# Performance work log

Measured on AMD Instinct MI355X. Metric: run time of the kernel, lower is better.

The kernel has to match this reference:

```python
import jax, jax.numpy as jnp
import numpy as np

B, S, D, E, T = 16, 128, 128, 64, 128  # batch, seq_len, token_dim, dep_dim, transformed_dim (T==D required by mask broadcast)
V_TOK, V_DEP = 100000, 64
DEPTH = 2


def setup_inputs() -> dict:
    key = jax.random.key(0)
    ks = jax.random.split(key, 12)
    return {
        "token_table": jax.random.normal(ks[0], (V_TOK, D), jnp.float32) * 0.1,
        "dep_table": jax.random.normal(ks[1], (V_DEP, E), jnp.float32) * 0.1,
        # Bilinear(D, E, T): weight [T, D, E], bias [T]
        "W1": jax.random.normal(ks[2], (T, D, E), jnp.float32) * 0.05,
        "b1": jax.random.normal(ks[3], (T,), jnp.float32) * 0.05,
        # Bilinear(D, T, D): weight [D, D, T], bias [D]
        "W2": jax.random.normal(ks[4], (D, D, T), jnp.float32) * 0.05,
        "b2": jax.random.normal(ks[5], (D,), jnp.float32) * 0.05,
        # Linear(S, 1): weight [S] (flattened [1,S]), bias [1]
        "wr": jax.random.normal(ks[6], (S,), jnp.float32) * 0.05,
        "br": jax.random.normal(ks[7], (1,), jnp.float32) * 0.05,
        "tokens": jax.random.randint(ks[8], (B, S), 0, V_TOK),
        "dep_types": jax.random.randint(ks[9], (B, S), 0, V_DEP),
        "dep_heads": jax.random.randint(ks[10], (B, S), 0, S),
    }


def _block(tok, dep_emb, heads, W1, b1, W2, b2, wr, br):
    # tok: [B,S,D], dep_emb: [B,S,E], heads: [B,S] with values in [0,S)
    b, s, d = tok.shape
    # dep_transform (Bilinear) + mask + tanh. Masked structure: full tensor
    # tde_full[b,i,j,:] = tde[b,j,:] if heads[b,j]==i else 0 (heads<S always here),
    # and tanh(0)=0, so only the i==heads[b,j] rows are nonzero after activation.
    tde = jnp.tanh(jnp.einsum('bsd,tde,bse->bst', tok, W1, dep_emb) + b1)  # [B,S,T]
    # composition bilinear at the nonzero (i==head) positions
    c_nz = jnp.tanh(jnp.einsum('bsd,pdt,bst->bsp', tok, W2, tde) + b2)    # [B,S,D]
    # at masked positions tde_full==0 -> composition output is tanh(bias)
    c_bg = jnp.tanh(b2)                                                   # [D]
    # reduction Linear(S,1): out[b,i,:] = sum_j wr[j]*c[b,i,j,:] + br
    base = jnp.sum(wr) * c_bg + br                                        # [D]
    delta = wr[None, :, None] * (c_nz - c_bg)                             # [B,S,D]
    seg = (jnp.arange(b)[:, None] * s + heads).reshape(-1)                # scatter target i=heads[b,j]
    scat = jax.ops.segment_sum(delta.reshape(b * s, d), seg, num_segments=b * s)
    return base + scat.reshape(b, s, d)


def reference(token_table, dep_table, W1, b1, W2, b2, wr, br, tokens, dep_types, dep_heads):
    tok = token_table[tokens]          # [B,S,D]
    dep = dep_table[dep_types]         # [B,S,E]
    for _ in range(DEPTH):
        tok = _block(tok, dep, dep_heads, W1, b1, W2, b2, wr, br)
    out_mask = (dep_heads == 0)[..., None].astype(tok.dtype)  # keep only root tokens
    return tok * out_mask
```

## Files before the change

### kernel.cpp

```cpp
#include <hip/hip_runtime.h>
#include <hip/hip_bf16.h>

#define BB 16
#define SS 128
#define DD 128
#define EE 64
#define TT 128
#define NN (BB*SS)
#define KSPLIT 16

typedef __attribute__((ext_vector_type(8))) short short8;
typedef __attribute__((ext_vector_type(4))) float f32x4;
typedef __attribute__((ext_vector_type(4))) unsigned int u32x4;

__device__ inline unsigned pkbf16(float a, float b) {
    unsigned r;
    asm volatile("v_cvt_pk_bf16_f32 %0, %1, %2" : "=v"(r) : "v"(a), "v"(b));
    return r;
}
__device__ inline float bflo(unsigned u) { return __builtin_bit_cast(float, (unsigned)(u << 16)); }
__device__ inline float bfhi(unsigned u) { return __builtin_bit_cast(float, (unsigned)(u & 0xffff0000u)); }

#define LDS_SWZ(row, bcol) ((row) * 256 + ((bcol) ^ (((row) & 7) << 4)))

__global__ __launch_bounds__(256) void k_prep1(const float* __restrict__ W1,
                                               const float* __restrict__ dep_table,
                                               const float* __restrict__ W2,
                                               const float* __restrict__ b2,
                                               const float* __restrict__ wr,
                                               const float* __restrict__ br,
                                               __hip_bfloat16* __restrict__ G1,
                                               __hip_bfloat16* __restrict__ W2b,
                                               float* __restrict__ basics) {
    int bid = blockIdx.x;
    int tid = threadIdx.x;
    if (bid < 512) {
        int bx = bid & 63, by = bid >> 6;
        int td = bx * 256 + tid;
        int v0 = by * 8;
        const float* w1row = W1 + (size_t)td * 64;
        float acc[8] = {};
#pragma unroll
        for (int e0 = 0; e0 < 64; e0 += 8) {
            f32x4 wa = *(const f32x4*)(w1row + e0);
            f32x4 wb = *(const f32x4*)(w1row + e0 + 4);
#pragma unroll
            for (int v = 0; v < 8; v++) {
                const float* dr = dep_table + (v0 + v) * 64 + e0;
                acc[v] += wa[0] * dr[0] + wa[1] * dr[1] + wa[2] * dr[2] + wa[3] * dr[3]
                        + wb[0] * dr[4] + wb[1] * dr[5] + wb[2] * dr[6] + wb[3] * dr[7];
            }
        }
#pragma unroll
        for (int v = 0; v < 8; v++)
            G1[(size_t)(v0 + v) * (TT * DD) + td] = __float2bfloat16(acc[v]);
    } else if (bid < 1536) {
        int cid = (bid - 512) * 256 + tid;
        int d = cid >> 11;
        int rem = cid & 2047;
        int p = rem >> 4;
        int sp = rem & 15;
        int h = sp >> 3, s = sp & 7;
        int t0 = h * 64 + ((s ^ (p & 7))) * 8;
        const float* src = W2 + ((size_t)p * 128 + d) * 128 + t0;
        f32x4 a = *(const f32x4*)(src);
        f32x4 b = *(const f32x4*)(src + 4);
        u32x4 o;
        o[0] = pkbf16(a[0], a[1]);
        o[1] = pkbf16(a[2], a[3]);
        o[2] = pkbf16(b[0], b[1]);
        o[3] = pkbf16(b[2], b[3]);
        *(u32x4*)((char*)W2b + (size_t)cid * 16) = o;
    } else {
        __shared__ float red[128];
        int t = tid;
        if (t < 128) red[t] = wr[t];
        __syncthreads();
        for (int s = 64; s > 0; s >>= 1) {
            if (t < s) red[t] += red[t + s];
            __syncthreads();
        }
        if (t < 128) {
            float swr = red[0];
            float cbg = tanhf(b2[t]);
            basics[t] = cbg;
            basics[128 + t] = swr * cbg + br[0];
        }
    }
}

__global__ __launch_bounds__(256) void k_prep2(const float* __restrict__ token_table,
                                               const int* __restrict__ tokens,
                                               const int* __restrict__ dep_types,
                                               const float* __restrict__ b1,
                                               const __hip_bfloat16* __restrict__ G1,
                                               float* __restrict__ tok,
                                               float* __restrict__ tde) {
    __shared__ float rows[2][128];
    int tid = threadIdx.x;
    int gid = blockIdx.x * 256 + tid;
    int n = gid >> 7, t = tid & 127, half = tid >> 7;
    float val = token_table[(size_t)tokens[n] * 128 + t];
    tok[gid] = val;
    rows[half][t] = val;
    __syncthreads();
    int v = dep_types[n];
    const unsigned* g = (const unsigned*)(G1 + (size_t)v * (TT * DD) + t * 128);
    const float* row = rows[half];
    float acc = b1[t];
#pragma unroll
    for (int i = 0; i < 16; i++) {
        u32x4 w = *(const u32x4*)(g + i * 4);
        acc += row[i * 8 + 0] * bflo(w[0]) + row[i * 8 + 1] * bfhi(w[0]);
        acc += row[i * 8 + 2] * bflo(w[1]) + row[i * 8 + 3] * bfhi(w[1]);
        acc += row[i * 8 + 4] * bflo(w[2]) + row[i * 8 + 5] * bfhi(w[2]);
        acc += row[i * 8 + 6] * bflo(w[3]) + row[i * 8 + 7] * bfhi(w[3]);
    }
    tde[(size_t)n * 128 + t] = tanhf(acc);
}

__global__ __launch_bounds__(256, 4) void k_gemm(const float* __restrict__ tok,
                                                 const float* __restrict__ tde,
                                                 const __hip_bfloat16* __restrict__ W2b,
                                                 float* __restrict__ part) {
    __shared__ char As[8192];
    __shared__ char Bs[32768];
    int id = blockIdx.x;
    int g = id & 7;
    int rblk = id >> 3;
    int ks = g * 2 + (rblk & 1);
    int nb = rblk >> 1;
    int tid = threadIdx.x;
    int lane = tid & 63, w = tid >> 6;
    int n0 = nb * 32, d0 = ks * 8;
    int lrow = lane & 15, lk = lane >> 4;
    int r = tid >> 3, o = tid & 7;
    int wbase16 = (tid & 192) * 16;

    f32x4 acc[2][2] = {};

    for (int dd = 0; dd < 8; dd++) {
        int d = d0 + dd;
        const char* bsrc = (const char*)W2b + (size_t)d * 32768;
#pragma unroll
        for (int i = 0; i < 8; i++) {
            __builtin_amdgcn_global_load_lds(
                (const __attribute__((address_space(1))) void*)(bsrc + (i * 256 + tid) * 16),
                (__attribute__((address_space(3))) void*)(Bs + i * 4096 + wbase16),
                16, 0, 0);
        }
        float tokv = tok[(size_t)(n0 + r) * 128 + d];
        const float* trow = tde + (size_t)(n0 + r) * 128 + o * 16;
        f32x4 xa = *(const f32x4*)(trow);
        f32x4 xb = *(const f32x4*)(trow + 4);
        f32x4 ya = *(const f32x4*)(trow + 8);
        f32x4 yb = *(const f32x4*)(trow + 12);
        u32x4 v0, v1;
        v0[0] = pkbf16(xa[0] * tokv, xa[1] * tokv);
        v0[1] = pkbf16(xa[2] * tokv, xa[3] * tokv);
        v0[2] = pkbf16(xb[0] * tokv, xb[1] * tokv);
        v0[3] = pkbf16(xb[2] * tokv, xb[3] * tokv);
        v1[0] = pkbf16(ya[0] * tokv, ya[1] * tokv);
        v1[1] = pkbf16(ya[2] * tokv, ya[3] * tokv);
        v1[2] = pkbf16(yb[0] * tokv, yb[1] * tokv);
        v1[3] = pkbf16(yb[2] * tokv, yb[3] * tokv);
        *(u32x4*)(As + LDS_SWZ(r, o * 32))      = v0;
        *(u32x4*)(As + LDS_SWZ(r, o * 32 + 16)) = v1;
        __syncthreads();
#pragma unroll
        for (int kk = 0; kk < 4; kk++) {
            short8 aF[2], bF[2];
#pragma unroll
            for (int mi = 0; mi < 2; mi++)
                aF[mi] = *(const short8*)(As + LDS_SWZ(mi * 16 + lrow, kk * 64 + lk * 16));
#pragma unroll
            for (int pj = 0; pj < 2; pj++)
                bF[pj] = *(const short8*)(Bs + LDS_SWZ(w * 32 + pj * 16 + lrow, kk * 64 + lk * 16));
#pragma unroll
            for (int mi = 0; mi < 2; mi++)
#pragma unroll
                for (int pj = 0; pj < 2; pj++)
                    acc[mi][pj] = __builtin_amdgcn_mfma_f32_16x16x32_bf16(
                        aF[mi], bF[pj], acc[mi][pj], 0, 0, 0);
        }
        __syncthreads();
    }
    float* pout = part + (size_t)ks * NN * 128;
#pragma unroll
    for (int mi = 0; mi < 2; mi++)
#pragma unroll
        for (int pj = 0; pj < 2; pj++)
#pragma unroll
            for (int rr = 0; rr < 4; rr++) {
                int row = mi * 16 + (lane >> 4) * 4 + rr;
                int col = w * 32 + pj * 16 + (lane & 15);
                pout[(size_t)(n0 + row) * 128 + col] = acc[mi][pj][rr];
            }
}

__global__ void k_e2a(const float* __restrict__ part, const int* __restrict__ heads,
                      const float* __restrict__ basics, const float* __restrict__ wr,
                      const float* __restrict__ b2, const int* __restrict__ dep_types,
                      const float* __restrict__ b1, const __hip_bfloat16* __restrict__ G1,
                      float* __restrict__ tok, float* __restrict__ tde) {
    int bi = blockIdx.x;
    int b = bi >> 7, i = bi & 127;
    int p = threadIdx.x;
    __shared__ int hs[128];
    __shared__ float row[128];
    hs[p] = heads[b * 128 + p];
    __syncthreads();
    float cbg = basics[p];
    float acc = basics[128 + p];
    for (int j = 0; j < 128; j++) {
        if (hs[j] == i) {
            int gg = (b * 128 + j) * 128 + p;
            float s = 0.f;
#pragma unroll
            for (int k = 0; k < KSPLIT; k++) s += part[(size_t)k * NN * 128 + gg];
            float c = tanhf(s + b2[p]);
            acc += wr[j] * (c - cbg);
        }
    }
    tok[(size_t)bi * 128 + p] = acc;
    row[p] = acc;
    __syncthreads();
    int v = dep_types[bi];
    const unsigned* g = (const unsigned*)(G1 + (size_t)v * (TT * DD) + p * 128);
    float a2 = b1[p];
#pragma unroll
    for (int ii = 0; ii < 16; ii++) {
        u32x4 w = *(const u32x4*)(g + ii * 4);
        a2 += row[ii * 8 + 0] * bflo(w[0]) + row[ii * 8 + 1] * bfhi(w[0]);
        a2 += row[ii * 8 + 2] * bflo(w[1]) + row[ii * 8 + 3] * bfhi(w[1]);
        a2 += row[ii * 8 + 4] * bflo(w[2]) + row[ii * 8 + 5] * bfhi(w[2]);
        a2 += row[ii * 8 + 6] * bflo(w[3]) + row[ii * 8 + 7] * bfhi(w[3]);
    }
    tde[(size_t)bi * 128 + p] = tanhf(a2);
}

__global__ void k_e2b(const float* __restrict__ part, const int* __restrict__ heads,
                      const float* __restrict__ basics, const float* __restrict__ wr,
                      const float* __restrict__ b2, float* __restrict__ out) {
    int bi = blockIdx.x;
    int b = bi >> 7, i = bi & 127;
    int p = threadIdx.x;
    __shared__ int hs[128];
    hs[p] = heads[b * 128 + p];
    __syncthreads();
    if (hs[i] != 0) {
        out[(size_t)bi * 128 + p] = 0.f;
        return;
    }
    float cbg = basics[p];
    float acc = basics[128 + p];
    for (int j = 0; j < 128; j++) {
        if (hs[j] == i) {
            int gg = (b * 128 + j) * 128 + p;
            float s = 0.f;
#pragma unroll
            for (int k = 0; k < KSPLIT; k++) s += part[(size_t)k * NN * 128 + gg];
            float c = tanhf(s + b2[p]);
            acc += wr[j] * (c - cbg);
        }
    }
    out[(size_t)bi * 128 + p] = acc;
}

extern "C" void kernel_launch(void* const* d_in, const int* in_sizes, int n_in,
                              void* d_out, int out_size, void* d_ws, size_t ws_size,
                              hipStream_t stream) {
    const float* token_table = (const float*)d_in[0];
    const float* dep_table   = (const float*)d_in[1];
    const float* W1          = (const float*)d_in[2];
    const float* b1          = (const float*)d_in[3];
    const float* W2          = (const float*)d_in[4];
    const float* b2          = (const float*)d_in[5];
    const float* wr          = (const float*)d_in[6];
    const float* br          = (const float*)d_in[7];
    const int* tokens        = (const int*)d_in[8];
    const int* dep_types     = (const int*)d_in[9];
    const int* dep_heads     = (const int*)d_in[10];
    float* out = (float*)d_out;

    char* ws = (char*)d_ws;
    __hip_bfloat16* G1  = (__hip_bfloat16*)(ws);
    __hip_bfloat16* W2b = (__hip_bfloat16*)(ws + (2ull << 20));
    float* tok    = (float*)(ws + (6ull << 20));
    float* tde    = (float*)(ws + (7ull << 20));
    float* part   = (float*)(ws + (9ull << 20));
    float* basics = (float*)(ws + (25ull << 20));

    k_prep1<<<1537, 256, 0, stream>>>(W1, dep_table, W2, b2, wr, br, G1, W2b, basics);
    k_prep2<<<1024, 256, 0, stream>>>(token_table, tokens, dep_types, b1, G1, tok, tde);

    k_gemm<<<1024, 256, 0, stream>>>(tok, tde, W2b, part);
    k_e2a<<<NN, 128, 0, stream>>>(part, dep_heads, basics, wr, b2,
                                  dep_types, b1, G1, tok, tde);
    k_gemm<<<1024, 256, 0, stream>>>(tok, tde, W2b, part);
    k_e2b<<<NN, 128, 0, stream>>>(part, dep_heads, basics, wr, b2, out);
}
```

Before: 105.0 us.

## Drop LDS staging in composition GEMM; load MFMA fragments directly from pre-permuted weights

The W2 bf16 repack is changed to write weights in MFMA-fragment order, so each lane loads its B operand with one contiguous 16-byte global load. The GEMM kernel no longer stages A and B through shared memory or uses barriers. Each wave keeps its tde rows in registers and builds the A fragments itself by scaling them with the token value. The block-to-tile mapping is also simplified. This removes LDS traffic and __syncthreads, but every wave now reads its B fragments straight from global memory or cache, and the extra tde registers may lower occupancy.

```diff
diff --git a/kernel.cpp b/kernel.cpp
--- a/kernel.cpp
+++ b/kernel.cpp
@@ -20,8 +20,6 @@
 }
 __device__ inline float bflo(unsigned u) { return __builtin_bit_cast(float, (unsigned)(u << 16)); }
 __device__ inline float bfhi(unsigned u) { return __builtin_bit_cast(float, (unsigned)(u & 0xffff0000u)); }
-
-#define LDS_SWZ(row, bcol) ((row) * 256 + ((bcol) ^ (((row) & 7) << 4)))
 
 __global__ __launch_bounds__(256) void k_prep1(const float* __restrict__ W1,
                                                const float* __restrict__ dep_table,
@@ -56,12 +54,12 @@
             G1[(size_t)(v0 + v) * (TT * DD) + td] = __float2bfloat16(acc[v]);
     } else if (bid < 1536) {
         int cid = (bid - 512) * 256 + tid;
-        int d = cid >> 11;
-        int rem = cid & 2047;
-        int p = rem >> 4;
-        int sp = rem & 15;
-        int h = sp >> 3, s = sp & 7;
-        int t0 = h * 64 + ((s ^ (p & 7))) * 8;
+        int l  = cid & 63;
+        int pf = (cid >> 6) & 7;
+        int kk = (cid >> 9) & 3;
+        int d  = cid >> 11;
+        int p  = pf * 16 + (l & 15);
+        int t0 = kk * 32 + (l >> 4) * 8;
         const float* src = W2 + ((size_t)p * 128 + d) * 128 + t0;
         f32x4 a = *(const f32x4*)(src);
         f32x4 b = *(const f32x4*)(src + 4);
@@ -123,67 +121,54 @@
                                                  const float* __restrict__ tde,
                                                  const __hip_bfloat16* __restrict__ W2b,
                                                  float* __restrict__ part) {
-    __shared__ char As[8192];
-    __shared__ char Bs[32768];
-    int id = blockIdx.x;
-    int g = id & 7;
-    int rblk = id >> 3;
-    int ks = g * 2 + (rblk & 1);
-    int nb = rblk >> 1;
     int tid = threadIdx.x;
-    int lane = tid & 63, w = tid >> 6;
-    int n0 = nb * 32, d0 = ks * 8;
-    int lrow = lane & 15, lk = lane >> 4;
-    int r = tid >> 3, o = tid & 7;
-    int wbase16 = (tid & 192) * 16;
+    int w = tid >> 6, lane = tid & 63;
+    int nt = blockIdx.x & 63, ks = blockIdx.x >> 6;
+    int n0 = nt * 32, d0 = ks * 8;
+    int lr = lane & 15, lk = lane >> 4;
+
+    f32x4 ta[2][4], tb[2][4];
+#pragma unroll
+    for (int mi = 0; mi < 2; mi++) {
+        const float* base = tde + (size_t)(n0 + mi * 16 + lr) * 128 + lk * 8;
+#pragma unroll
+        for (int kk = 0; kk < 4; kk++) {
+            ta[mi][kk] = *(const f32x4*)(base + kk * 32);
+            tb[mi][kk] = *(const f32x4*)(base + kk * 32 + 4);
+        }
+    }
+    const float* tokp0 = tok + (size_t)(n0 + lr) * 128 + d0;
+    const float* tokp1 = tok + (size_t)(n0 + 16 + lr) * 128 + d0;
 
     f32x4 acc[2][2] = {};
-
+    const char* wb = (const char*)W2b;
+
+#pragma unroll 2
     for (int dd = 0; dd < 8; dd++) {
         int d = d0 + dd;
-        const char* bsrc = (const char*)W2b + (size_t)d * 32768;
-#pragma unroll
-        for (int i = 0; i < 8; i++) {
-            __builtin_amdgcn_global_load_lds(
-                (const __attribute__((address_space(1))) void*)(bsrc + (i * 256 + tid) * 16),
-                (__attribute__((address_space(3))) void*)(Bs + i * 4096 + wbase16),
-                16, 0, 0);
-        }
-        float tokv = tok[(size_t)(n0 + r) * 128 + d];
-        const float* trow = tde + (size_t)(n0 + r) * 128 + o * 16;
-        f32x4 xa = *(const f32x4*)(trow);
-        f32x4 xb = *(const f32x4*)(trow + 4);
-        f32x4 ya = *(const f32x4*)(trow + 8);
-        f32x4 yb = *(const f32x4*)(trow + 12);
-        u32x4 v0, v1;
-        v0[0] = pkbf16(xa[0] * tokv, xa[1] * tokv);
-        v0[1] = pkbf16(xa[2] * tokv, xa[3] * tokv);
-        v0[2] = pkbf16(xb[0] * tokv, xb[1] * tokv);
-        v0[3] = pkbf16(xb[2] * tokv, xb[3] * tokv);
-        v1[0] = pkbf16(ya[0] * tokv, ya[1] * tokv);
-        v1[1] = pkbf16(ya[2] * tokv, ya[3] * tokv);
-        v1[2] = pkbf16(yb[0] * tokv, yb[1] * tokv);
-        v1[3] = pkbf16(yb[2] * tokv, yb[3] * tokv);
-        *(u32x4*)(As + LDS_SWZ(r, o * 32))      = v0;
-        *(u32x4*)(As + LDS_SWZ(r, o * 32 + 16)) = v1;
-        __syncthreads();
+        float tv0 = tokp0[dd];
+        float tv1 = tokp1[dd];
 #pragma unroll
         for (int kk = 0; kk < 4; kk++) {
-            short8 aF[2], bF[2];
-#pragma unroll
-            for (int mi = 0; mi < 2; mi++)
-                aF[mi] = *(const short8*)(As + LDS_SWZ(mi * 16 + lrow, kk * 64 + lk * 16));
-#pragma unroll
-            for (int pj = 0; pj < 2; pj++)
-                bF[pj] = *(const short8*)(Bs + LDS_SWZ(w * 32 + pj * 16 + lrow, kk * 64 + lk * 16));
-#pragma unroll
-            for (int mi = 0; mi < 2; mi++)
-#pragma unroll
-                for (int pj = 0; pj < 2; pj++)
-                    acc[mi][pj] = __builtin_amdgcn_mfma_f32_16x16x32_bf16(
-                        aF[mi], bF[pj], acc[mi][pj], 0, 0, 0);
-        }
-        __syncthreads();
+            size_t cb = ((size_t)(d * 4 + kk) * 8 + w * 2) * 64 + lane;
+            short8 bF0 = *(const short8*)(wb + cb * 16);
+            short8 bF1 = *(const short8*)(wb + (cb + 64) * 16);
+            u32x4 u0, u1;
+            u0[0] = pkbf16(ta[0][kk][0] * tv0, ta[0][kk][1] * tv0);
+            u0[1] = pkbf16(ta[0][kk][2] * tv0, ta[0][kk][3] * tv0);
+            u0[2] = pkbf16(tb[0][kk][0] * tv0, tb[0][kk][1] * tv0);
+            u0[3] = pkbf16(tb[0][kk][2] * tv0, tb[0][kk][3] * tv0);
+            u1[0] = pkbf16(ta[1][kk][0] * tv1, ta[1][kk][1] * tv1);
+            u1[1] = pkbf16(ta[1][kk][2] * tv1, ta[1][kk][3] * tv1);
+            u1[2] = pkbf16(tb[1][kk][0] * tv1, tb[1][kk][1] * tv1);
+            u1[3] = pkbf16(tb[1][kk][2] * tv1, tb[1][kk][3] * tv1);
+            short8 aF0 = __builtin_bit_cast(short8, u0);
+            short8 aF1 = __builtin_bit_cast(short8, u1);
+            acc[0][0] = __builtin_amdgcn_mfma_f32_16x16x32_bf16(aF0, bF0, acc[0][0], 0, 0, 0);
+            acc[0][1] = __builtin_amdgcn_mfma_f32_16x16x32_bf16(aF0, bF1, acc[0][1], 0, 0, 0);
+            acc[1][0] = __builtin_amdgcn_mfma_f32_16x16x32_bf16(aF1, bF0, acc[1][0], 0, 0, 0);
+            acc[1][1] = __builtin_amdgcn_mfma_f32_16x16x32_bf16(aF1, bF1, acc[1][1], 0, 0, 0);
+        }
     }
     float* pout = part + (size_t)ks * NN * 128;
 #pragma unroll
```

Measured after the change: 116.3 us. 1.11x slower.
